# Optimization experiments

Hardware: AMD Instinct MI355X
Metric: run time of the kernel (lower is better)

Reference implementation:

```python
import jax, jax.numpy as jnp
import numpy as np

L, B, S, H, NH, FF = 4, 16, 512, 768, 12, 3072
D = H // NH
SCALE = D ** -0.5
EPS = 1e-5


def _ln(x, g, b):
    m = jnp.mean(x, axis=-1, keepdims=True)
    v = jnp.mean((x - m) ** 2, axis=-1, keepdims=True)
    return (x - m) * jax.lax.rsqrt(v + EPS) * g + b


def setup_inputs() -> dict:
    key = jax.random.key(0)
    ks = jax.random.split(key, 16)
    def n(k, shape, s=0.02):
        return jax.random.normal(k, shape, dtype=jnp.float32) * s
    return {
        "x": jax.random.normal(ks[0], (B, S, H), dtype=jnp.float32),
        "attn_bias": jax.random.normal(ks[1], (B, NH, S, S), dtype=jnp.float32) * 0.1,
        "ln1_g": jnp.ones((L, H), jnp.float32), "ln1_b": jnp.zeros((L, H), jnp.float32),
        "wq": n(ks[2], (L, H, H)), "bq": jnp.zeros((L, H), jnp.float32),
        "wk": n(ks[3], (L, H, H)), "bk": jnp.zeros((L, H), jnp.float32),
        "wv": n(ks[4], (L, H, H)), "bv": jnp.zeros((L, H), jnp.float32),
        "wo": n(ks[5], (L, H, H)), "bo": jnp.zeros((L, H), jnp.float32),
        "ln2_g": jnp.ones((L, H), jnp.float32), "ln2_b": jnp.zeros((L, H), jnp.float32),
        "w1": n(ks[6], (L, H, FF)), "b1": jnp.zeros((L, FF), jnp.float32),
        "w2": n(ks[7], (L, FF, H)), "b2": jnp.zeros((L, H), jnp.float32),
        "fln_g": jnp.ones((H,), jnp.float32), "fln_b": jnp.zeros((H,), jnp.float32),
    }


def reference(x, attn_bias, ln1_g, ln1_b, wq, bq, wk, bk, wv, bv, wo, bo,
              ln2_g, ln2_b, w1, b1, w2, b2, fln_g, fln_b):
    def body(h, p):
        l1g, l1b, Wq, Bq, Wk, Bk, Wv, Bv, Wo, Bo, l2g, l2b, W1, B1, W2, B2 = p
        y = _ln(h, l1g, l1b)
        # [B,S,H] -> [B,NH,S,D]
        q = (y @ Wq + Bq).reshape(B, S, NH, D).transpose(0, 2, 1, 3)
        k = (y @ Wk + Bk).reshape(B, S, NH, D).transpose(0, 2, 1, 3)
        v = (y @ Wv + Bv).reshape(B, S, NH, D).transpose(0, 2, 1, 3)
        a = jnp.einsum('bhsd,bhtd->bhst', q * SCALE, k) + attn_bias
        a = jax.nn.softmax(a, axis=-1)
        o = jnp.einsum('bhst,bhtd->bhsd', a, v).transpose(0, 2, 1, 3).reshape(B, S, H)
        h = h + o @ Wo + Bo
        y = _ln(h, l2g, l2b)
        y = jax.nn.gelu(y @ W1 + B1, approximate=False) @ W2 + B2
        return h + y, None

    params = (ln1_g, ln1_b, wq, bq, wk, bk, wv, bv, wo, bo, ln2_g, ln2_b, w1, b1, w2, b2)
    x, _ = jax.lax.scan(body, x, params)
    return _ln(x, fln_g, fln_b)
```

## Files before the change

kernel.cpp:

```cpp
#include <hip/hip_runtime.h>
#include <math.h>

constexpr int Lc = 4, Bc = 16, Sc = 512, Hc = 768, NHc = 12, FFc = 3072, Dc = 64;
constexpr int MR = Bc * Sc;
constexpr int QS = 2304;
constexpr float SCALEc = 0.125f;

typedef __attribute__((ext_vector_type(8))) __bf16 bf16x8;
typedef __attribute__((ext_vector_type(4))) __bf16 bf16x4;
typedef __attribute__((ext_vector_type(4))) float  floatx4;

__device__ inline floatx4 mfma16(bf16x8 a, bf16x8 b, floatx4 c) {
    return __builtin_amdgcn_mfma_f32_16x16x32_bf16(a, b, c, 0, 0, 0);
}
__device__ inline float gelu_f(float x) {
    return 0.5f * x * (1.0f + erff(x * 0.70710678118654752f));
}
__device__ inline void ld16(const __bf16* g, __bf16* l) {
    __builtin_amdgcn_global_load_lds(
        (const __attribute__((address_space(1))) void*)g,
        (__attribute__((address_space(3))) void*)l, 16, 0, 0);
}

template<bool FINAL>
__global__ __launch_bounds__(256) void ln_k(
    const float* __restrict__ x, const float* __restrict__ g, const float* __restrict__ bt,
    __bf16* __restrict__ yb, float* __restrict__ yf)
{
    const int row  = blockIdx.x * 4 + (threadIdx.x >> 6);
    const int lane = threadIdx.x & 63;
    const int col  = lane * 12;
    const float* xr = x + (size_t)row * Hc + col;
    float v[12];
    *(float4*)(v + 0) = *(const float4*)(xr + 0);
    *(float4*)(v + 4) = *(const float4*)(xr + 4);
    *(float4*)(v + 8) = *(const float4*)(xr + 8);
    float s = 0.f, s2 = 0.f;
#pragma unroll
    for (int j = 0; j < 12; ++j) { s += v[j]; s2 += v[j] * v[j]; }
#pragma unroll
    for (int o = 32; o > 0; o >>= 1) { s += __shfl_xor(s, o); s2 += __shfl_xor(s2, o); }
    const float mean = s * (1.0f / Hc);
    const float inv  = rsqrtf(s2 * (1.0f / Hc) - mean * mean + 1e-5f);
    float gv[12], bv[12];
    *(float4*)(gv + 0) = *(const float4*)(g + col);
    *(float4*)(gv + 4) = *(const float4*)(g + col + 4);
    *(float4*)(gv + 8) = *(const float4*)(g + col + 8);
    *(float4*)(bv + 0) = *(const float4*)(bt + col);
    *(float4*)(bv + 4) = *(const float4*)(bt + col + 4);
    *(float4*)(bv + 8) = *(const float4*)(bt + col + 8);
    if (FINAL) {
        float o[12];
#pragma unroll
        for (int j = 0; j < 12; ++j) o[j] = (v[j] - mean) * inv * gv[j] + bv[j];
        float* yr = yf + (size_t)row * Hc + col;
        *(float4*)(yr + 0) = *(float4*)(o + 0);
        *(float4*)(yr + 4) = *(float4*)(o + 4);
        *(float4*)(yr + 8) = *(float4*)(o + 8);
    } else {
        __bf16 o[12];
#pragma unroll
        for (int j = 0; j < 12; ++j) o[j] = (__bf16)((v[j] - mean) * inv * gv[j] + bv[j]);
        __bf16* yr = yb + (size_t)row * Hc + col;
        *(bf16x4*)(yr + 0) = *(bf16x4*)(o + 0);
        *(bf16x4*)(yr + 4) = *(bf16x4*)(o + 4);
        *(bf16x4*)(yr + 8) = *(bf16x4*)(o + 8);
    }
}

__global__ __launch_bounds__(256) void prep_k(
    const float* __restrict__ wq, const float* __restrict__ wk,
    const float* __restrict__ wv, const float* __restrict__ wo,
    const float* __restrict__ w1, const float* __restrict__ w2,
    const float* __restrict__ bq, const float* __restrict__ bk, const float* __restrict__ bv,
    __bf16* __restrict__ wqkvt, __bf16* __restrict__ wot,
    __bf16* __restrict__ w1t, __bf16* __restrict__ w2t, float* __restrict__ bqkv)
{
    const int id = blockIdx.x;
    if (id >= 6912) {
        int i = (id - 6912) * 256 + threadIdx.x;
        if (i < QS) bqkv[i] = i < Hc ? bq[i] : (i < 2 * Hc ? bk[i - Hc] : bv[i - 2 * Hc]);
        return;
    }
    const float* in; __bf16* out; int R, C, tile;
    if (id < 2304) {
        int piece = id / 576; tile = id % 576; R = Hc; C = Hc;
        in  = piece == 0 ? wq : piece == 1 ? wk : piece == 2 ? wv : wo;
        out = piece == 3 ? wot : wqkvt + (size_t)piece * Hc * Hc;
    } else if (id < 4608) {
        tile = id - 2304; R = Hc; C = FFc; in = w1; out = w1t;
    } else {
        tile = id - 4608; R = FFc; C = Hc; in = w2; out = w2t;
    }
    const int nx = C / 32;
    const int bx = tile % nx, by = tile / nx;
    __shared__ float t[32][33];
    const int c0 = bx * 32, r0 = by * 32;
    const int tx = threadIdx.x & 31, ty = threadIdx.x >> 5;
#pragma unroll
    for (int i2 = 0; i2 < 4; ++i2)
        t[ty + i2 * 8][tx] = in[(size_t)(r0 + ty + i2 * 8) * C + c0 + tx];
    __syncthreads();
#pragma unroll
    for (int i2 = 0; i2 < 4; ++i2)
        out[(size_t)(c0 + ty + i2 * 8) * R + r0 + tx] = (__bf16)t[tx][ty + i2 * 8];
}

template<int ACT, bool RESID>
__global__ __launch_bounds__(256) void gemm2_k(
    const __bf16* __restrict__ A, const __bf16* __restrict__ Bt,
    const float* __restrict__ bias, const float* __restrict__ resid,
    float* __restrict__ outF, __bf16* __restrict__ outB,
    int M, int N, int K)
{
    __shared__ alignas(16) __bf16 As[128 * 32];
    __shared__ alignas(16) __bf16 Bs[128 * 32];
    const int tid  = threadIdx.x;
    const int wave = tid >> 6, lane = tid & 63, lhi = lane >> 4, llo = lane & 15;
    const int wm = wave >> 1, wn = wave & 1;
    const int row0 = blockIdx.y * 128, col0 = blockIdx.x * 128;
    const int srow = lane >> 2;
    const int scol = (lane & 3) * 8;

    floatx4 acc[4][4];
#pragma unroll
    for (int i = 0; i < 4; ++i)
#pragma unroll
        for (int j = 0; j < 4; ++j) acc[i][j] = {0.f, 0.f, 0.f, 0.f};

    const __bf16* Ab = A  + (size_t)(row0 + wave * 16 + srow) * K + scol;
    const __bf16* Bb = Bt + (size_t)(col0 + wave * 16 + srow) * K + scol;

    for (int kt = 0; kt < K; kt += 32) {
#pragma unroll
        for (int t = 0; t < 2; ++t) {
            ld16(Ab + (size_t)(t * 64) * K + kt, As + (t * 64 + wave * 16) * 32);
            ld16(Bb + (size_t)(t * 64) * K + kt, Bs + (t * 64 + wave * 16) * 32);
        }
        __syncthreads();
        bf16x8 af[4], bfr[4];
#pragma unroll
        for (int i = 0; i < 4; ++i)
            af[i]  = *(const bf16x8*)(As + (wm * 64 + i * 16 + llo) * 32 + lhi * 8);
#pragma unroll
        for (int j = 0; j < 4; ++j)
            bfr[j] = *(const bf16x8*)(Bs + (wn * 64 + j * 16 + llo) * 32 + lhi * 8);
#pragma unroll
        for (int i = 0; i < 4; ++i)
#pragma unroll
            for (int j = 0; j < 4; ++j)
                acc[i][j] = mfma16(af[i], bfr[j], acc[i][j]);
        __syncthreads();
    }
#pragma unroll
    for (int i = 0; i < 4; ++i) {
#pragma unroll
        for (int j = 0; j < 4; ++j) {
            int colc = col0 + wn * 64 + j * 16 + llo;
            float bb = bias[colc];
#pragma unroll
            for (int r = 0; r < 4; ++r) {
                int rowc = row0 + wm * 64 + i * 16 + lhi * 4 + r;
                float vv = acc[i][j][r] + bb;
                if (ACT == 1) vv = gelu_f(vv);
                size_t idx = (size_t)rowc * N + colc;
                if (RESID) outF[idx] = resid[idx] + vv;
                else       outB[idx] = (__bf16)vv;
            }
        }
    }
}

__global__ __launch_bounds__(128) void gemm3_k(
    const __bf16* __restrict__ A, const __bf16* __restrict__ Bt,
    const float* __restrict__ bias, const float* __restrict__ resid,
    float* __restrict__ outF, int M, int N, int K)
{
    __shared__ alignas(16) __bf16 As[128 * 32];
    __shared__ alignas(16) __bf16 Bs[64 * 32];
    const int tid  = threadIdx.x;
    const int wave = tid >> 6, lane = tid & 63, lhi = lane >> 4, llo = lane & 15;
    const int row0 = blockIdx.y * 128, col0 = blockIdx.x * 64;
    const int srow = lane >> 2;
    const int scol = (lane & 3) * 8;

    floatx4 acc[4][4];
#pragma unroll
    for (int i = 0; i < 4; ++i)
#pragma unroll
        for (int j = 0; j < 4; ++j) acc[i][j] = {0.f, 0.f, 0.f, 0.f};

    const __bf16* Ab = A  + (size_t)(row0 + wave * 64 + srow) * K + scol;
    const __bf16* Bb = Bt + (size_t)(col0 + wave * 32 + srow) * K + scol;

    for (int kt = 0; kt < K; kt += 32) {
#pragma unroll
        for (int t = 0; t < 4; ++t)
            ld16(Ab + (size_t)(t * 16) * K + kt, As + (wave * 64 + t * 16) * 32);
#pragma unroll
        for (int t = 0; t < 2; ++t)
            ld16(Bb + (size_t)(t * 16) * K + kt, Bs + (wave * 32 + t * 16) * 32);
        __syncthreads();
        bf16x8 af[4], bfr[4];
#pragma unroll
        for (int i = 0; i < 4; ++i)
            af[i]  = *(const bf16x8*)(As + (wave * 64 + i * 16 + llo) * 32 + lhi * 8);
#pragma unroll
        for (int j = 0; j < 4; ++j)
            bfr[j] = *(const bf16x8*)(Bs + (j * 16 + llo) * 32 + lhi * 8);
#pragma unroll
        for (int i = 0; i < 4; ++i)
#pragma unroll
            for (int j = 0; j < 4; ++j)
                acc[i][j] = mfma16(af[i], bfr[j], acc[i][j]);
        __syncthreads();
    }
#pragma unroll
    for (int i = 0; i < 4; ++i) {
#pragma unroll
        for (int j = 0; j < 4; ++j) {
            int colc = col0 + j * 16 + llo;
            float bb = bias[colc];
#pragma unroll
            for (int r = 0; r < 4; ++r) {
                int rowc = row0 + wave * 64 + i * 16 + lhi * 4 + r;
                size_t idx = (size_t)rowc * N + colc;
                outF[idx] = resid[idx] + acc[i][j][r] + bb;
            }
        }
    }
}

__global__ __launch_bounds__(256) void attn_k(
    const __bf16* __restrict__ q, const __bf16* __restrict__ k,
    const __bf16* __restrict__ v, const float* __restrict__ bias,
    __bf16* __restrict__ o)
{
    __shared__ alignas(16) __bf16 QPs[64][72];
    __shared__ alignas(16) __bf16 Ks[2][64][72];
    __shared__ alignas(16) __bf16 Vt[2][64][66];

    const int hh = blockIdx.x % NHc, b = blockIdx.x / NHc, qt = blockIdx.y;
    const int tid = threadIdx.x, wave = tid >> 6, lane = tid & 63;
    const int lhi = lane >> 4, llo = lane & 15;
    const size_t base  = (size_t)b * Sc * QS + hh * Dc;
    const size_t obase = (size_t)b * Sc * Hc + hh * Dc;

    const int sr0 = tid >> 3;
    const int sc0 = (tid & 7) * 8;

    {
        bf16x8 q0 = *(const bf16x8*)(q + base + (size_t)(qt * 64 + sr0) * QS + sc0);
        bf16x8 q1 = *(const bf16x8*)(q + base + (size_t)(qt * 64 + sr0 + 32) * QS + sc0);
        *(bf16x8*)(&QPs[sr0][sc0])      = q0;
        *(bf16x8*)(&QPs[sr0 + 32][sc0]) = q1;
        bf16x8 k0 = *(const bf16x8*)(k + base + (size_t)(sr0) * QS + sc0);
        bf16x8 k1 = *(const bf16x8*)(k + base + (size_t)(sr0 + 32) * QS + sc0);
        *(bf16x8*)(&Ks[0][sr0][sc0])      = k0;
        *(bf16x8*)(&Ks[0][sr0 + 32][sc0]) = k1;
        bf16x8 v0 = *(const bf16x8*)(v + base + (size_t)(sr0) * QS + sc0);
        bf16x8 v1 = *(const bf16x8*)(v + base + (size_t)(sr0 + 32) * QS + sc0);
#pragma unroll
        for (int jj = 0; jj < 8; ++jj) {
            Vt[0][sc0 + jj][sr0]      = v0[jj];
            Vt[0][sc0 + jj][sr0 + 32] = v1[jj];
        }
    }
    __syncthreads();

    bf16x8 aq0 = *(const bf16x8*)(&QPs[wave * 16 + llo][0 * 32 + lhi * 8]);
    bf16x8 aq1 = *(const bf16x8*)(&QPs[wave * 16 + llo][1 * 32 + lhi * 8]);

    float m_reg[4], l_reg[4];
#pragma unroll
    for (int r = 0; r < 4; ++r) { m_reg[r] = -1e30f; l_reg[r] = 0.f; }

    floatx4 acco[4];
#pragma unroll
    for (int j = 0; j < 4; ++j) acco[j] = {0.f, 0.f, 0.f, 0.f};

    const float* brow = bias + ((size_t)(b * NHc + hh) * Sc + qt * 64) * Sc;

    float bnx[4][4];
#pragma unroll
    for (int nf = 0; nf < 4; ++nf)
#pragma unroll
        for (int r = 0; r < 4; ++r)
            bnx[nf][r] = brow[(size_t)(wave * 16 + lhi * 4 + r) * Sc + nf * 16 + llo];

    for (int it = 0; it < 8; ++it) {
        const int cur = it & 1;
        bf16x8 k0, k1, v0, v1;
        if (it < 7) {
            const int ktn = (it + 1) * 64;
            k0 = *(const bf16x8*)(k + base + (size_t)(ktn + sr0) * QS + sc0);
            k1 = *(const bf16x8*)(k + base + (size_t)(ktn + sr0 + 32) * QS + sc0);
            v0 = *(const bf16x8*)(v + base + (size_t)(ktn + sr0) * QS + sc0);
            v1 = *(const bf16x8*)(v + base + (size_t)(ktn + sr0 + 32) * QS + sc0);
        }
        floatx4 accs[4];
#pragma unroll
        for (int j = 0; j < 4; ++j) accs[j] = {0.f, 0.f, 0.f, 0.f};
#pragma unroll
        for (int nf = 0; nf < 4; ++nf) {
            bf16x8 bk2 = *(const bf16x8*)(&Ks[cur][nf * 16 + llo][lhi * 8]);
            accs[nf] = mfma16(aq0, bk2, accs[nf]);
        }
#pragma unroll
        for (int nf = 0; nf < 4; ++nf) {
            bf16x8 bk2 = *(const bf16x8*)(&Ks[cur][nf * 16 + llo][32 + lhi * 8]);
            accs[nf] = mfma16(aq1, bk2, accs[nf]);
        }
        float sv[4][4];
#pragma unroll
        for (int nf = 0; nf < 4; ++nf)
#pragma unroll
            for (int r = 0; r < 4; ++r)
                sv[nf][r] = accs[nf][r] * SCALEc + bnx[nf][r];
        if (it < 7) {
            const int ktn = (it + 1) * 64;
#pragma unroll
            for (int nf = 0; nf < 4; ++nf)
#pragma unroll
                for (int r = 0; r < 4; ++r)
                    bnx[nf][r] = brow[(size_t)(wave * 16 + lhi * 4 + r) * Sc + ktn + nf * 16 + llo];
        }
        float al[4];
#pragma unroll
        for (int r = 0; r < 4; ++r) {
            float mx = fmaxf(fmaxf(sv[0][r], sv[1][r]), fmaxf(sv[2][r], sv[3][r]));
            mx = fmaxf(mx, __shfl_xor(mx, 1));
            mx = fmaxf(mx, __shfl_xor(mx, 2));
            mx = fmaxf(mx, __shfl_xor(mx, 4));
            mx = fmaxf(mx, __shfl_xor(mx, 8));
            float mnew = fmaxf(m_reg[r], mx);
            al[r] = __expf(m_reg[r] - mnew);
            m_reg[r] = mnew;
            float sum = 0.f;
#pragma unroll
            for (int nf = 0; nf < 4; ++nf) {
                float p = __expf(sv[nf][r] - mnew);
                sum += p;
                QPs[wave * 16 + lhi * 4 + r][nf * 16 + llo] = (__bf16)p;
            }
            sum += __shfl_xor(sum, 1);
            sum += __shfl_xor(sum, 2);
            sum += __shfl_xor(sum, 4);
            sum += __shfl_xor(sum, 8);
            l_reg[r] = l_reg[r] * al[r] + sum;
        }
#pragma unroll
        for (int nf = 0; nf < 4; ++nf)
#pragma unroll
            for (int r = 0; r < 4; ++r) acco[nf][r] *= al[r];
#pragma unroll
        for (int kk = 0; kk < 2; ++kk) {
            bf16x8 ap = *(const bf16x8*)(&QPs[wave * 16 + llo][kk * 32 + lhi * 8]);
#pragma unroll
            for (int nf = 0; nf < 4; ++nf) {
                bf16x8 bv2 = *(const bf16x8*)(&Vt[cur][nf * 16 + llo][kk * 32 + lhi * 8]);
                acco[nf] = mfma16(ap, bv2, acco[nf]);
            }
        }
        if (it < 7) {
            *(bf16x8*)(&Ks[cur ^ 1][sr0][sc0])      = k0;
            *(bf16x8*)(&Ks[cur ^ 1][sr0 + 32][sc0]) = k1;
#pragma unroll
            for (int jj = 0; jj < 8; ++jj) {
                Vt[cur ^ 1][sc0 + jj][sr0]      = v0[jj];
                Vt[cur ^ 1][sc0 + jj][sr0 + 32] = v1[jj];
            }
        }
        __syncthreads();
    }
#pragma unroll
    for (int nf = 0; nf < 4; ++nf) {
#pragma unroll
        for (int r = 0; r < 4; ++r) {
            int lr = wave * 16 + lhi * 4 + r;
            float oo = acco[nf][r] / l_reg[r];
            o[obase + (size_t)(qt * 64 + lr) * Hc + nf * 16 + llo] = (__bf16)oo;
        }
    }
}

extern "C" void kernel_launch(void* const* d_in, const int* in_sizes, int n_in,
                              void* d_out, int out_size, void* d_ws, size_t ws_size,
                              hipStream_t stream)
{
    const float* x     = (const float*)d_in[0];
    const float* abias = (const float*)d_in[1];
    const float* ln1g  = (const float*)d_in[2];
    const float* ln1b  = (const float*)d_in[3];
    const float* wq    = (const float*)d_in[4];
    const float* bq    = (const float*)d_in[5];
    const float* wk    = (const float*)d_in[6];
    const float* bk    = (const float*)d_in[7];
    const float* wv    = (const float*)d_in[8];
    const float* bv    = (const float*)d_in[9];
    const float* wo    = (const float*)d_in[10];
    const float* bo    = (const float*)d_in[11];
    const float* ln2g  = (const float*)d_in[12];
    const float* ln2b  = (const float*)d_in[13];
    const float* w1    = (const float*)d_in[14];
    const float* b1    = (const float*)d_in[15];
    const float* w2    = (const float*)d_in[16];
    const float* b2    = (const float*)d_in[17];
    const float* flng  = (const float*)d_in[18];
    const float* flnb  = (const float*)d_in[19];

    float* h = (float*)d_out;
    __bf16* y    = (__bf16*)d_ws;
    __bf16* qkv  = y   + (size_t)MR * Hc;
    __bf16* ob   = qkv + (size_t)MR * QS;
    __bf16* fb   = ob  + (size_t)MR * Hc;
    __bf16* w1t  = fb  + (size_t)MR * FFc;
    __bf16* w2t  = w1t + (size_t)FFc * Hc;
    float*  bqkv = (float*)(w2t + (size_t)Hc * FFc);
    __bf16* wqkvt = fb;
    __bf16* wot   = fb + (size_t)QS * Hc;

    hipMemcpyAsync(h, x, (size_t)MR * Hc * sizeof(float), hipMemcpyDeviceToDevice, stream);

    dim3 blk(256);
    dim3 gLN(MR / 4);
    dim3 gQKV(QS / 128, MR / 128);
    dim3 gP64(Hc / 64, MR / 128);
    dim3 gF(FFc / 128, MR / 128);
    dim3 gA(Bc * NHc, Sc / 64);
    dim3 gPrep(6921);

    for (int l = 0; l < Lc; ++l) {
        const float* wq_l = wq + (size_t)l * Hc * Hc;
        const float* wk_l = wk + (size_t)l * Hc * Hc;
        const float* wv_l = wv + (size_t)l * Hc * Hc;
        const float* wo_l = wo + (size_t)l * Hc * Hc;
        const float* w1_l = w1 + (size_t)l * Hc * FFc;
        const float* w2_l = w2 + (size_t)l * FFc * Hc;

        prep_k<<<gPrep, blk, 0, stream>>>(wq_l, wk_l, wv_l, wo_l, w1_l, w2_l,
                                          bq + l * Hc, bk + l * Hc, bv + l * Hc,
                                          wqkvt, wot, w1t, w2t, bqkv);

        ln_k<false><<<gLN, blk, 0, stream>>>(h, ln1g + l * Hc, ln1b + l * Hc, y, nullptr);
        gemm2_k<0, false><<<gQKV, blk, 0, stream>>>(y, wqkvt, bqkv, nullptr, nullptr, qkv, MR, QS, Hc);
        attn_k<<<gA, blk, 0, stream>>>(qkv, qkv + Hc, qkv + 2 * Hc, abias, ob);
        gemm3_k<<<gP64, dim3(128), 0, stream>>>(ob, wot, bo + l * Hc, h, h, MR, Hc, Hc);
        ln_k<false><<<gLN, blk, 0, stream>>>(h, ln2g + l * Hc, ln2b + l * Hc, y, nullptr);
        gemm2_k<1, false><<<gF, blk, 0, stream>>>(y, w1t, b1 + l * FFc, nullptr, nullptr, fb, MR, FFc, Hc);
        gemm3_k<<<gP64, dim3(128), 0, stream>>>(fb, w2t, b2 + l * Hc, h, h, MR, Hc, FFc);
    }
    ln_k<true><<<gLN, blk, 0, stream>>>(h, flng, flnb, nullptr, h);
}
```

Measured before the change: 1.662 ms.

## Split K across wave pairs in residual GEMM with LDS reduction

The 128x64-tile residual GEMM goes from 2 to 4 waves (256 threads). Each pair of waves handles half of the K dimension in its own LDS buffers, and the two partial accumulators are summed through an LDS scratch area before the bias and residual epilogue. The aim is more waves in flight per block to hide latency in the out-projection and FFN-down GEMMs. The cost is twice the LDS per block, an extra reduction pass, and an epilogue done by only half the waves.

```diff
diff --git a/kernel.cpp b/kernel.cpp
--- a/kernel.cpp
+++ b/kernel.cpp
@@ -171,18 +171,24 @@
     }
 }
 
-__global__ __launch_bounds__(128) void gemm3_k(
+__global__ __launch_bounds__(256) void gemm3_k(
     const __bf16* __restrict__ A, const __bf16* __restrict__ Bt,
     const float* __restrict__ bias, const float* __restrict__ resid,
     float* __restrict__ outF, int M, int N, int K)
 {
-    __shared__ alignas(16) __bf16 As[128 * 32];
-    __shared__ alignas(16) __bf16 Bs[64 * 32];
+    __shared__ alignas(16) unsigned char smem[33792];
+    __bf16* As = (__bf16*)smem;
+    __bf16* Bs = As + 2 * 128 * 32;
+    float*  Rs = (float*)smem;
+
     const int tid  = threadIdx.x;
     const int wave = tid >> 6, lane = tid & 63, lhi = lane >> 4, llo = lane & 15;
+    const int pair = wave >> 1;
+    const int wrow = wave & 1;
     const int row0 = blockIdx.y * 128, col0 = blockIdx.x * 64;
     const int srow = lane >> 2;
     const int scol = (lane & 3) * 8;
+    const int Kh   = K >> 1;
 
     floatx4 acc[4][4];
 #pragma unroll
@@ -190,24 +196,26 @@
 #pragma unroll
         for (int j = 0; j < 4; ++j) acc[i][j] = {0.f, 0.f, 0.f, 0.f};
 
-    const __bf16* Ab = A  + (size_t)(row0 + wave * 64 + srow) * K + scol;
-    const __bf16* Bb = Bt + (size_t)(col0 + wave * 32 + srow) * K + scol;
-
-    for (int kt = 0; kt < K; kt += 32) {
+    const __bf16* Ab = A  + (size_t)(row0 + wrow * 64 + srow) * K + (size_t)pair * Kh + scol;
+    const __bf16* Bb = Bt + (size_t)(col0 + wrow * 32 + srow) * K + (size_t)pair * Kh + scol;
+    __bf16* AsP = As + pair * (128 * 32);
+    __bf16* BsP = Bs + pair * (64 * 32);
+
+    for (int kt = 0; kt < Kh; kt += 32) {
 #pragma unroll
         for (int t = 0; t < 4; ++t)
-            ld16(Ab + (size_t)(t * 16) * K + kt, As + (wave * 64 + t * 16) * 32);
+            ld16(Ab + (size_t)(t * 16) * K + kt, AsP + (wrow * 64 + t * 16) * 32);
 #pragma unroll
         for (int t = 0; t < 2; ++t)
-            ld16(Bb + (size_t)(t * 16) * K + kt, Bs + (wave * 32 + t * 16) * 32);
+            ld16(Bb + (size_t)(t * 16) * K + kt, BsP + (wrow * 32 + t * 16) * 32);
         __syncthreads();
         bf16x8 af[4], bfr[4];
 #pragma unroll
         for (int i = 0; i < 4; ++i)
-            af[i]  = *(const bf16x8*)(As + (wave * 64 + i * 16 + llo) * 32 + lhi * 8);
+            af[i]  = *(const bf16x8*)(AsP + (wrow * 64 + i * 16 + llo) * 32 + lhi * 8);
 #pragma unroll
         for (int j = 0; j < 4; ++j)
-            bfr[j] = *(const bf16x8*)(Bs + (j * 16 + llo) * 32 + lhi * 8);
+            bfr[j] = *(const bf16x8*)(BsP + (j * 16 + llo) * 32 + lhi * 8);
 #pragma unroll
         for (int i = 0; i < 4; ++i)
 #pragma unroll
@@ -215,17 +223,32 @@
                 acc[i][j] = mfma16(af[i], bfr[j], acc[i][j]);
         __syncthreads();
     }
-#pragma unroll
-    for (int i = 0; i < 4; ++i) {
-#pragma unroll
-        for (int j = 0; j < 4; ++j) {
-            int colc = col0 + j * 16 + llo;
-            float bb = bias[colc];
-#pragma unroll
-            for (int r = 0; r < 4; ++r) {
-                int rowc = row0 + wave * 64 + i * 16 + lhi * 4 + r;
-                size_t idx = (size_t)rowc * N + colc;
-                outF[idx] = resid[idx] + acc[i][j][r] + bb;
+
+    if (pair == 1) {
+#pragma unroll
+        for (int i = 0; i < 4; ++i)
+#pragma unroll
+            for (int j = 0; j < 4; ++j)
+#pragma unroll
+                for (int r = 0; r < 4; ++r)
+                    Rs[(wrow * 64 + i * 16 + lhi * 4 + r) * 66 + j * 16 + llo] = acc[i][j][r];
+    }
+    __syncthreads();
+    if (pair == 0) {
+#pragma unroll
+        for (int i = 0; i < 4; ++i) {
+#pragma unroll
+            for (int j = 0; j < 4; ++j) {
+                int colc = col0 + j * 16 + llo;
+                float bb = bias[colc];
+#pragma unroll
+                for (int r = 0; r < 4; ++r) {
+                    int rloc = wrow * 64 + i * 16 + lhi * 4 + r;
+                    int rowc = row0 + rloc;
+                    float vv = acc[i][j][r] + Rs[rloc * 66 + j * 16 + llo] + bb;
+                    size_t idx = (size_t)rowc * N + colc;
+                    outF[idx] = resid[idx] + vv;
+                }
             }
         }
     }
@@ -445,10 +468,10 @@
         ln_k<false><<<gLN, blk, 0, stream>>>(h, ln1g + l * Hc, ln1b + l * Hc, y, nullptr);
         gemm2_k<0, false><<<gQKV, blk, 0, stream>>>(y, wqkvt, bqkv, nullptr, nullptr, qkv, MR, QS, Hc);
         attn_k<<<gA, blk, 0, stream>>>(qkv, qkv + Hc, qkv + 2 * Hc, abias, ob);
-        gemm3_k<<<gP64, dim3(128), 0, stream>>>(ob, wot, bo + l * Hc, h, h, MR, Hc, Hc);
+        gemm3_k<<<gP64, blk, 0, stream>>>(ob, wot, bo + l * Hc, h, h, MR, Hc, Hc);
         ln_k<false><<<gLN, blk, 0, stream>>>(h, ln2g + l * Hc, ln2b + l * Hc, y, nullptr);
         gemm2_k<1, false><<<gF, blk, 0, stream>>>(y, w1t, b1 + l * FFc, nullptr, nullptr, fb, MR, FFc, Hc);
-        gemm3_k<<<gP64, dim3(128), 0, stream>>>(fb, w2t, b2 + l * Hc, h, h, MR, Hc, FFc);
+        gemm3_k<<<gP64, blk, 0, stream>>>(fb, w2t, b2 + l * Hc, h, h, MR, Hc, FFc);
     }
     ln_k<true><<<gLN, blk, 0, stream>>>(h, flng, flnb, nullptr, h);
 }
```

Measured after the change: 1.755 ms. +5.6%, slower.

## Double-buffer gemm3 LDS tiles and use four waves per block

Applied to the files above, without the earlier changes.

The output-projection and FFN-down GEMM kernel now runs 256 threads (4 waves), each covering 32 rows instead of 64, and double-buffers the A/B LDS tiles so the next k-slice loads while MFMAs run on the current one. This is meant to hide global-to-LDS latency and raise wave-level parallelism for these N=768 GEMMs. In exchange each wave holds fewer accumulators and reuses each B fragment less, LDS use doubles, and one barrier per iteration is dropped.

```diff
diff --git a/kernel.cpp b/kernel.cpp
--- a/kernel.cpp
+++ b/kernel.cpp
@@ -171,59 +171,66 @@
     }
 }
 
-__global__ __launch_bounds__(128) void gemm3_k(
+__global__ __launch_bounds__(256) void gemm3_k(
     const __bf16* __restrict__ A, const __bf16* __restrict__ Bt,
     const float* __restrict__ bias, const float* __restrict__ resid,
     float* __restrict__ outF, int M, int N, int K)
 {
-    __shared__ alignas(16) __bf16 As[128 * 32];
-    __shared__ alignas(16) __bf16 Bs[64 * 32];
+    __shared__ alignas(16) __bf16 As[2][128 * 32];
+    __shared__ alignas(16) __bf16 Bs[2][64 * 32];
     const int tid  = threadIdx.x;
     const int wave = tid >> 6, lane = tid & 63, lhi = lane >> 4, llo = lane & 15;
     const int row0 = blockIdx.y * 128, col0 = blockIdx.x * 64;
     const int srow = lane >> 2;
     const int scol = (lane & 3) * 8;
 
-    floatx4 acc[4][4];
-#pragma unroll
-    for (int i = 0; i < 4; ++i)
+    floatx4 acc[2][4];
+#pragma unroll
+    for (int i = 0; i < 2; ++i)
 #pragma unroll
         for (int j = 0; j < 4; ++j) acc[i][j] = {0.f, 0.f, 0.f, 0.f};
 
-    const __bf16* Ab = A  + (size_t)(row0 + wave * 64 + srow) * K + scol;
-    const __bf16* Bb = Bt + (size_t)(col0 + wave * 32 + srow) * K + scol;
-
-    for (int kt = 0; kt < K; kt += 32) {
-#pragma unroll
-        for (int t = 0; t < 4; ++t)
-            ld16(Ab + (size_t)(t * 16) * K + kt, As + (wave * 64 + t * 16) * 32);
-#pragma unroll
-        for (int t = 0; t < 2; ++t)
-            ld16(Bb + (size_t)(t * 16) * K + kt, Bs + (wave * 32 + t * 16) * 32);
-        __syncthreads();
-        bf16x8 af[4], bfr[4];
-#pragma unroll
-        for (int i = 0; i < 4; ++i)
-            af[i]  = *(const bf16x8*)(As + (wave * 64 + i * 16 + llo) * 32 + lhi * 8);
+    const __bf16* Ab = A  + (size_t)(row0 + wave * 32 + srow) * K + scol;
+    const __bf16* Bb = Bt + (size_t)(col0 + wave * 16 + srow) * K + scol;
+
+#define G3_STAGE(buf, kt)                                                      \
+    do {                                                                       \
+        ld16(Ab + (kt),                   &As[buf][(wave * 32 +  0) * 32]);    \
+        ld16(Ab + (size_t)16 * K + (kt),  &As[buf][(wave * 32 + 16) * 32]);    \
+        ld16(Bb + (kt),                   &Bs[buf][(wave * 16) * 32]);         \
+    } while (0)
+
+    G3_STAGE(0, 0);
+    __syncthreads();
+    const int nt = K >> 5;
+    for (int t = 0; t < nt; ++t) {
+        const int cur = t & 1;
+        if (t + 1 < nt) G3_STAGE(cur ^ 1, (size_t)(t + 1) * 32);
+        bf16x8 af[2], bfr[4];
+#pragma unroll
+        for (int i = 0; i < 2; ++i)
+            af[i]  = *(const bf16x8*)(&As[cur][(wave * 32 + i * 16 + llo) * 32 + lhi * 8]);
 #pragma unroll
         for (int j = 0; j < 4; ++j)
-            bfr[j] = *(const bf16x8*)(Bs + (j * 16 + llo) * 32 + lhi * 8);
-#pragma unroll
-        for (int i = 0; i < 4; ++i)
+            bfr[j] = *(const bf16x8*)(&Bs[cur][(j * 16 + llo) * 32 + lhi * 8]);
+#pragma unroll
+        for (int i = 0; i < 2; ++i)
 #pragma unroll
             for (int j = 0; j < 4; ++j)
                 acc[i][j] = mfma16(af[i], bfr[j], acc[i][j]);
         __syncthreads();
     }
-#pragma unroll
-    for (int i = 0; i < 4; ++i) {
+#undef G3_STAGE
+
+#pragma unroll
+    for (int i = 0; i < 2; ++i) {
 #pragma unroll
         for (int j = 0; j < 4; ++j) {
             int colc = col0 + j * 16 + llo;
             float bb = bias[colc];
 #pragma unroll
             for (int r = 0; r < 4; ++r) {
-                int rowc = row0 + wave * 64 + i * 16 + lhi * 4 + r;
+                int rowc = row0 + wave * 32 + i * 16 + lhi * 4 + r;
                 size_t idx = (size_t)rowc * N + colc;
                 outF[idx] = resid[idx] + acc[i][j][r] + bb;
             }
@@ -445,10 +452,10 @@
         ln_k<false><<<gLN, blk, 0, stream>>>(h, ln1g + l * Hc, ln1b + l * Hc, y, nullptr);
         gemm2_k<0, false><<<gQKV, blk, 0, stream>>>(y, wqkvt, bqkv, nullptr, nullptr, qkv, MR, QS, Hc);
         attn_k<<<gA, blk, 0, stream>>>(qkv, qkv + Hc, qkv + 2 * Hc, abias, ob);
-        gemm3_k<<<gP64, dim3(128), 0, stream>>>(ob, wot, bo + l * Hc, h, h, MR, Hc, Hc);
+        gemm3_k<<<gP64, blk, 0, stream>>>(ob, wot, bo + l * Hc, h, h, MR, Hc, Hc);
         ln_k<false><<<gLN, blk, 0, stream>>>(h, ln2g + l * Hc, ln2b + l * Hc, y, nullptr);
         gemm2_k<1, false><<<gF, blk, 0, stream>>>(y, w1t, b1 + l * FFc, nullptr, nullptr, fb, MR, FFc, Hc);
-        gemm3_k<<<gP64, dim3(128), 0, stream>>>(fb, w2t, b2 + l * Hc, h, h, MR, Hc, FFc);
+        gemm3_k<<<gP64, blk, 0, stream>>>(fb, w2t, b2 + l * Hc, h, h, MR, Hc, FFc);
     }
     ln_k<true><<<gLN, blk, 0, stream>>>(h, flng, flnb, nullptr, h);
 }
```

Result: faster. 1.625 ms (-2.2%).
